# Performance work log

Measured on AMD Instinct MI355X. Metric: run time of the kernel, lower is better.

Reference implementation:

```python
import jax, jax.numpy as jnp
import numpy as np

D_MODEL = 1024
N_HEADS = 16
D_K = D_MODEL // N_HEADS
RANK = 16
LORA_SCALING = 32.0 / RANK  # alpha / rank = 2.0
LN_EPS = 1e-5


def _lora_linear(x, w, b, A, B):
    # torch nn.Linear: x @ w.T + b ; LoRA: (x @ A @ B) * scaling
    return x @ w.T + b + (x @ A @ B) * LORA_SCALING


def setup_inputs() -> dict:
    key = jax.random.key(0)
    ks = jax.random.split(key, 20)
    d = {}
    d['x'] = jax.random.normal(ks[0], (4, 1024, D_MODEL), dtype=jnp.float32)
    i = 1
    for p in ('q', 'k', 'v', 'o'):
        d[f'{p}_w'] = jax.random.normal(ks[i], (D_MODEL, D_MODEL), dtype=jnp.float32) * (1.0 / np.sqrt(D_MODEL)); i += 1
        d[f'{p}_b'] = jax.random.normal(ks[i], (D_MODEL,), dtype=jnp.float32) * 0.01; i += 1
        d[f'{p}_A'] = jax.random.normal(ks[i], (D_MODEL, RANK), dtype=jnp.float32) * 0.01; i += 1
        d[f'{p}_B'] = jax.random.normal(ks[i], (RANK, D_MODEL), dtype=jnp.float32) * 0.01; i += 1
    d['ln_g'] = jnp.ones((D_MODEL,), dtype=jnp.float32)
    d['ln_b'] = jnp.zeros((D_MODEL,), dtype=jnp.float32)
    return d


def reference(x, q_w, q_b, q_A, q_B, k_w, k_b, k_A, k_B,
              v_w, v_b, v_A, v_B, o_w, o_b, o_A, o_B, ln_g, ln_b):
    B, S, _ = x.shape
    # QKV projections with LoRA, reshape to [B, H, S, d_k]
    def split_heads(t):
        return t.reshape(B, S, N_HEADS, D_K).transpose(0, 2, 1, 3)
    Q = split_heads(_lora_linear(x, q_w, q_b, q_A, q_B))
    K = split_heads(_lora_linear(x, k_w, k_b, k_A, k_B))
    V = split_heads(_lora_linear(x, v_w, v_b, v_A, v_B))

    scores = jnp.einsum('bhqd,bhkd->bhqk', Q, K) / jnp.sqrt(jnp.float32(D_K))
    attn = jax.nn.softmax(scores, axis=-1)  # dropout is identity in eval
    ctx = jnp.einsum('bhqk,bhkd->bhqd', attn, V)
    ctx = ctx.transpose(0, 2, 1, 3).reshape(B, S, D_MODEL)

    out = _lora_linear(ctx, o_w, o_b, o_A, o_B)
    # residual + LayerNorm
    h = out + x
    mu = jnp.mean(h, axis=-1, keepdims=True)
    var = jnp.mean(jnp.square(h - mu), axis=-1, keepdims=True)
    normed = (h - mu) * jax.lax.rsqrt(var + LN_EPS) * ln_g + ln_b
    return normed, attn.mean(axis=1)
```

## Files before the change

### kernel.cpp

```cpp
#include <hip/hip_runtime.h>

#define DMODEL 1024
#define NHEADS 16
#define DHEAD  64
#define RANK   16
#define BATCH  4
#define SEQ    1024
#define MTOT   (BATCH*SEQ)
#define QSCALE 0.18033688011112042f

typedef __bf16 bf16;
typedef __bf16 bf16x8 __attribute__((ext_vector_type(8)));
typedef __bf16 bf16x4 __attribute__((ext_vector_type(4)));
typedef float  f32x4  __attribute__((ext_vector_type(4)));

__device__ __forceinline__ int swz128(int row, int byte_in_row) {
  int slot = byte_in_row >> 4;
  return row * 128 + (((slot ^ (row & 7)) << 4) | (byte_in_row & 15));
}

__device__ __forceinline__ void gll16(const void* g, void* l) {
  __builtin_amdgcn_global_load_lds((const __attribute__((address_space(1))) unsigned int*)g,
                                   (__attribute__((address_space(3))) unsigned int*)l, 16, 0, 0);
}

#define TRRD(lo, hi, base, o0, o1)                                   \
  asm volatile("ds_read_b64_tr_b16 %0, %2 offset:" #o0 "\n\t"        \
               "ds_read_b64_tr_b16 %1, %2 offset:" #o1               \
               : "=v"(lo), "=v"(hi) : "v"(base));

__global__ void prep_weff_kernel(
    const float* __restrict__ W0, const float* __restrict__ A0, const float* __restrict__ B0,
    const float* __restrict__ W1, const float* __restrict__ A1, const float* __restrict__ B1,
    const float* __restrict__ W2, const float* __restrict__ A2, const float* __restrict__ B2,
    const float* __restrict__ W3, const float* __restrict__ A3, const float* __restrict__ B3,
    bf16* __restrict__ out) {
  const int l = blockIdx.y;
  const float* W = l == 0 ? W0 : l == 1 ? W1 : l == 2 ? W2 : W3;
  const float* A = l == 0 ? A0 : l == 1 ? A1 : l == 2 ? A2 : A3;
  const float* Bm = l == 0 ? B0 : l == 1 ? B1 : l == 2 ? B2 : B3;
  out += (size_t)l * DMODEL * DMODEL;
  const int n = blockIdx.x;
  __shared__ float bsc[RANK];
  if (threadIdx.x < RANK) bsc[threadIdx.x] = Bm[threadIdx.x * DMODEL + n] * 2.0f;
  __syncthreads();
  float br[RANK];
#pragma unroll
  for (int r = 0; r < RANK; ++r) br[r] = bsc[r];
  for (int k0 = 0; k0 < DMODEL; k0 += 256) {
    int k = k0 + threadIdx.x;
    float acc = W[n * DMODEL + k];
    const float4* arow = (const float4*)(A + k * RANK);
#pragma unroll
    for (int r4 = 0; r4 < 4; ++r4) {
      float4 a = arow[r4];
      acc += a.x*br[r4*4+0] + a.y*br[r4*4+1] + a.z*br[r4*4+2] + a.w*br[r4*4+3];
    }
    out[n * DMODEL + k] = (bf16)acc;
  }
}

__global__ void cast_x_kernel(const float* __restrict__ x, bf16* __restrict__ xb) {
  int i = (blockIdx.x * blockDim.x + threadIdx.x) * 4;
  float4 v = *(const float4*)(x + i);
  bf16x4 o = { (bf16)v.x, (bf16)v.y, (bf16)v.z, (bf16)v.w };
  *(bf16x4*)(xb + i) = o;
}

__global__ __launch_bounds__(512) void gemm_qkv_kernel(
    const bf16* __restrict__ xb, const bf16* __restrict__ weff,
    const float* __restrict__ bq, const float* __restrict__ bk, const float* __restrict__ bv,
    bf16* __restrict__ Qb, bf16* __restrict__ Kb, bf16* __restrict__ Vb)
{
  __shared__ __align__(16) char sA[16384];
  __shared__ __align__(16) char sB[32768];
  const int tid = threadIdx.x, w = tid >> 6, lane = tid & 63;
  const int bid = blockIdx.x;
  const int nb = (bid & 7) * 48 + (bid >> 3);
  const int n0 = (nb % 12) * 256, m0 = (nb / 12) * 128;
  const int z = n0 >> 10;
  const float* bias = z == 0 ? bq : z == 1 ? bk : bv;
  bf16* outp = z == 0 ? Qb : (z == 1 ? Kb : Vb);
  const float scl = z == 0 ? QSCALE : 1.0f;
  const int wm = (w & 1) * 64, wn = (w >> 1) * 64;
  f32x4 acc[4][4] = {};

  const bf16* pA[2]; const bf16* pB[4]; char* lA[2]; char* lB[4];
#pragma unroll
  for (int i = 0; i < 2; ++i) {
    int ci = i * 8 + w;
    int row = ci * 8 + (lane >> 3);
    int ss = (lane & 7) ^ (row & 7);
    pA[i] = xb + (size_t)(m0 + row) * DMODEL + ss * 8;
    lA[i] = sA + ci * 1024;
  }
#pragma unroll
  for (int i = 0; i < 4; ++i) {
    int ci = i * 8 + w;
    int row = ci * 8 + (lane >> 3);
    int ss = (lane & 7) ^ (row & 7);
    pB[i] = weff + (size_t)(n0 + row) * DMODEL + ss * 8;
    lB[i] = sB + ci * 1024;
  }
  for (int kt = 0; kt < DMODEL / 64; ++kt) {
    const int kbase = kt * 64;
#pragma unroll
    for (int i = 0; i < 2; ++i) gll16(pA[i] + kbase, lA[i]);
#pragma unroll
    for (int i = 0; i < 4; ++i) gll16(pB[i] + kbase, lB[i]);
    __syncthreads();
#pragma unroll
    for (int ks = 0; ks < 2; ++ks) {
      bf16x8 af[4], bfg[4];
#pragma unroll
      for (int mi = 0; mi < 4; ++mi)
        af[mi] = *(const bf16x8*)(sA + swz128(wm + mi*16 + (lane & 15), ks*64 + (lane >> 4)*16));
#pragma unroll
      for (int ni = 0; ni < 4; ++ni)
        bfg[ni] = *(const bf16x8*)(sB + swz128(wn + ni*16 + (lane & 15), ks*64 + (lane >> 4)*16));
#pragma unroll
      for (int mi = 0; mi < 4; ++mi)
#pragma unroll
        for (int ni = 0; ni < 4; ++ni)
          acc[mi][ni] = __builtin_amdgcn_mfma_f32_16x16x32_bf16(af[mi], bfg[ni], acc[mi][ni], 0, 0, 0);
    }
    __syncthreads();
  }

#pragma unroll
  for (int mi = 0; mi < 4; ++mi) {
#pragma unroll
    for (int ni = 0; ni < 4; ++ni) {
      int col = n0 + wn + ni * 16 + (lane & 15);
      float bcol = bias[col & 1023];
      int h = (col >> 6) & 15, d = col & 63;
#pragma unroll
      for (int r = 0; r < 4; ++r) {
        int row = m0 + wm + mi * 16 + (lane >> 4) * 4 + r;
        float v = (acc[mi][ni][r] + bcol) * scl;
        int b = row >> 10, s = row & 1023;
        outp[(size_t)((b * NHEADS + h) * SEQ + s) * DHEAD + d] = (bf16)v;
      }
    }
  }
}

__device__ __forceinline__ void gemm_core64(
    const bf16* __restrict__ Ain, const bf16* __restrict__ Bin,
    char* sA, char* sB, int m0, int n0, f32x4 (&acc)[2][4]) {
  const int tid = threadIdx.x;
  const int w = tid >> 6, lane = tid & 63;
  const int wm = (w & 1) * 32, wn = (w >> 1) * 64;
  const bf16* pA[2]; char* lA[2];
  const bf16* pB[4]; char* lB[4];
#pragma unroll
  for (int i = 0; i < 2; ++i) {
    int chunk = i * 4 + w;
    int row = chunk * 8 + (lane >> 3);
    int ss = (lane & 7) ^ (row & 7);
    pA[i] = Ain + (size_t)(m0 + row) * DMODEL + ss * 8;
    lA[i] = sA + chunk * 1024;
  }
#pragma unroll
  for (int i = 0; i < 4; ++i) {
    int chunk = i * 4 + w;
    int row = chunk * 8 + (lane >> 3);
    int ss = (lane & 7) ^ (row & 7);
    pB[i] = Bin + (size_t)(n0 + row) * DMODEL + ss * 8;
    lB[i] = sB + chunk * 1024;
  }
  for (int kt = 0; kt < DMODEL / 64; ++kt) {
    const int kbase = kt * 64;
#pragma unroll
    for (int i = 0; i < 2; ++i) gll16(pA[i] + kbase, lA[i]);
#pragma unroll
    for (int i = 0; i < 4; ++i) gll16(pB[i] + kbase, lB[i]);
    __syncthreads();
#pragma unroll
    for (int ks = 0; ks < 2; ++ks) {
      bf16x8 af[2], bfg[4];
#pragma unroll
      for (int mi = 0; mi < 2; ++mi)
        af[mi] = *(const bf16x8*)(sA + swz128(wm + mi*16 + (lane & 15), ks*64 + (lane >> 4)*16));
#pragma unroll
      for (int ni = 0; ni < 4; ++ni)
        bfg[ni] = *(const bf16x8*)(sB + swz128(wn + ni*16 + (lane & 15), ks*64 + (lane >> 4)*16));
#pragma unroll
      for (int mi = 0; mi < 2; ++mi)
#pragma unroll
        for (int ni = 0; ni < 4; ++ni)
          acc[mi][ni] = __builtin_amdgcn_mfma_f32_16x16x32_bf16(af[mi], bfg[ni], acc[mi][ni], 0, 0, 0);
    }
    __syncthreads();
  }
}

__global__ __launch_bounds__(256) void gemm_o_kernel(
    const bf16* __restrict__ ctx, const bf16* __restrict__ weff,
    const float* __restrict__ bias, const float* __restrict__ resid,
    float* __restrict__ outf)
{
  __shared__ __align__(16) char sA[8192];
  __shared__ __align__(16) char sB[16384];
  const int tid = threadIdx.x, w = tid >> 6, lane = tid & 63;
  const int bid = blockIdx.x;
  const int nb = (bid & 7) * 64 + (bid >> 3);
  const int n0 = (nb & 7) * 128, m0 = (nb >> 3) * 64;
  const int wm = (w & 1) * 32, wn = (w >> 1) * 64;
  f32x4 acc[2][4] = {};
  gemm_core64(ctx, weff, sA, sB, m0, n0, acc);
#pragma unroll
  for (int mi = 0; mi < 2; ++mi) {
#pragma unroll
    for (int ni = 0; ni < 4; ++ni) {
      int col = n0 + wn + ni * 16 + (lane & 15);
      float bcol = bias[col];
#pragma unroll
      for (int r = 0; r < 4; ++r) {
        int row = m0 + wm + mi * 16 + (lane >> 4) * 4 + r;
        outf[(size_t)row * DMODEL + col] =
            acc[mi][ni][r] + bcol + resid[(size_t)row * DMODEL + col];
      }
    }
  }
}

__global__ __launch_bounds__(512) void flash_kernel(
    const bf16* __restrict__ Qb, const bf16* __restrict__ Kb, const bf16* __restrict__ Vb,
    bf16* __restrict__ ctx, float* __restrict__ lstat)
{
  __shared__ __align__(16) char sK[2 * 8192];
  __shared__ __align__(16) char sV[2 * 8192];
  __shared__ __align__(16) char sP[8 * 2048];
  const int tid = threadIdx.x, w = tid >> 6, lane = tid & 63;
  const int bid = blockIdx.x;
  const int nb = (bid & 7) * 64 + (bid >> 3);
  const int bh = nb >> 3;
  const int q0 = (nb & 7) * 128;
  const bf16* Qbase = Qb + (size_t)bh * SEQ * DHEAD;
  const bf16* Kbase = Kb + (size_t)bh * SEQ * DHEAD;
  const bf16* Vbase = Vb + (size_t)bh * SEQ * DHEAD;
  const int qw = q0 + w * 16;

  bf16x8 aq[2];
#pragma unroll
  for (int ks = 0; ks < 2; ++ks)
    aq[ks] = *(const bf16x8*)(Qbase + (size_t)(qw + (lane & 15)) * DHEAD + ks * 32 + (lane >> 4) * 8);

  const bf16* pK; const bf16* pV; int lKo; int lVo;
  {
    int ci = w;
    int rowK = ci * 8 + (lane >> 3);
    int ssK = (lane & 7) ^ (rowK & 7);
    pK = Kbase + (size_t)rowK * DHEAD + ssK * 8;
    lKo = ci * 1024;
    int kV = ci * 8 + ((lane >> 5) & 1) * 4 + ((lane >> 1) & 3);
    int dV = (((lane >> 3) & 3) << 4) + ((lane & 1) << 3);
    pV = Vbase + (size_t)kV * DHEAD + dV;
    lVo = ci * 1024;
  }

  char* sPw = sP + w * 2048;
  const unsigned pbase = (unsigned)(uintptr_t)sPw + ((lane >> 4) << 8) + ((lane & 15) << 3);
  const unsigned vbase0 = (unsigned)(uintptr_t)sV + ((lane >> 4) << 10) + ((lane & 15) << 3);
  char* pwr = sPw + ((lane >> 4) << 3) + (lane & 15) * 32;

  f32x4 cacc[4] = {};
  float lsum[4] = {0.f, 0.f, 0.f, 0.f};

  gll16(pK, sK + lKo);
  gll16(pV, sV + lVo);
  __syncthreads();

  for (int kt = 0; kt < SEQ / 64; ++kt) {
    const int cur = (kt & 1) << 13, nxt = cur ^ 8192;
    if (kt + 1 < SEQ / 64) {
      const size_t kofs = (size_t)((kt + 1) * 64) * DHEAD;
      gll16(pK + kofs, sK + nxt + lKo);
      gll16(pV + kofs, sV + nxt + lVo);
    }

    f32x4 sc[4] = {};
#pragma unroll
    for (int ks = 0; ks < 2; ++ks)
#pragma unroll
      for (int ni = 0; ni < 4; ++ni) {
        bf16x8 bk = *(const bf16x8*)(sK + cur + swz128(ni*16 + (lane & 15), ks*64 + (lane >> 4)*16));
        sc[ni] = __builtin_amdgcn_mfma_f32_16x16x32_bf16(aq[ks], bk, sc[ni], 0, 0, 0);
      }

#pragma unroll
    for (int ni = 0; ni < 4; ++ni) {
      float p0 = __builtin_amdgcn_exp2f(sc[ni][0]);
      float p1 = __builtin_amdgcn_exp2f(sc[ni][1]);
      float p2 = __builtin_amdgcn_exp2f(sc[ni][2]);
      float p3 = __builtin_amdgcn_exp2f(sc[ni][3]);
      lsum[0] += p0; lsum[1] += p1; lsum[2] += p2; lsum[3] += p3;
      bf16x4 pb = { (bf16)p0, (bf16)p1, (bf16)p2, (bf16)p3 };
      *(bf16x4*)(pwr + ni * 512) = pb;
    }
    asm volatile("s_waitcnt lgkmcnt(0)" ::: "memory");

    unsigned long long t0, t1, v0[4], v1[4];
    const unsigned vb = vbase0 + cur;
    TRRD(t0, t1, pbase, 0, 128)
    TRRD(v0[0], v1[0], vb, 0, 512)
    TRRD(v0[1], v1[1], vb, 128, 640)
    TRRD(v0[2], v1[2], vb, 256, 768)
    TRRD(v0[3], v1[3], vb, 384, 896)
    asm volatile("s_waitcnt lgkmcnt(0)" ::: "memory");
    __builtin_amdgcn_sched_barrier(0);
    {
      union { unsigned long long u[2]; bf16x8 v; } pu, vu;
      pu.u[0] = t0; pu.u[1] = t1;
#pragma unroll
      for (int ni = 0; ni < 4; ++ni) {
        vu.u[0] = v0[ni]; vu.u[1] = v1[ni];
        cacc[ni] = __builtin_amdgcn_mfma_f32_16x16x32_bf16(pu.v, vu.v, cacc[ni], 0, 0, 0);
      }
    }
    TRRD(t0, t1, pbase, 1024, 1152)
    TRRD(v0[0], v1[0], vb, 4096, 4608)
    TRRD(v0[1], v1[1], vb, 4224, 4736)
    TRRD(v0[2], v1[2], vb, 4352, 4864)
    TRRD(v0[3], v1[3], vb, 4480, 4992)
    asm volatile("s_waitcnt lgkmcnt(0)" ::: "memory");
    __builtin_amdgcn_sched_barrier(0);
    {
      union { unsigned long long u[2]; bf16x8 v; } pu, vu;
      pu.u[0] = t0; pu.u[1] = t1;
#pragma unroll
      for (int ni = 0; ni < 4; ++ni) {
        vu.u[0] = v0[ni]; vu.u[1] = v1[ni];
        cacc[ni] = __builtin_amdgcn_mfma_f32_16x16x32_bf16(pu.v, vu.v, cacc[ni], 0, 0, 0);
      }
    }
    __syncthreads();
  }

#pragma unroll
  for (int r = 0; r < 4; ++r) {
#pragma unroll
    for (int off = 1; off < 16; off <<= 1) lsum[r] += __shfl_xor(lsum[r], off);
  }

  const int b = bh >> 4, hh = bh & 15;
#pragma unroll
  for (int r = 0; r < 4; ++r) {
    float inv = __builtin_amdgcn_rcpf(lsum[r]);
    int qrow = qw + (lane >> 4) * 4 + r;
#pragma unroll
    for (int ni = 0; ni < 4; ++ni) {
      int d = ni * 16 + (lane & 15);
      ctx[(size_t)(b * SEQ + qrow) * DMODEL + hh * DHEAD + d] = (bf16)(cacc[ni][r] * inv);
    }
    if ((lane & 15) == 0) lstat[(size_t)bh * SEQ + qrow] = lsum[r];
  }
}

__global__ __launch_bounds__(256) void mean_kernel(
    const bf16* __restrict__ Qb, const bf16* __restrict__ Kb,
    const float* __restrict__ lstat, float* __restrict__ out2)
{
  __shared__ __align__(16) char sK[2 * 16384];
  const int tid = threadIdx.x, w = tid >> 6, lane = tid & 63;
  const int bid = blockIdx.x;
  const int nb2 = (bid & 7) * 64 + (bid >> 3);
  const int b = nb2 >> 7;
  const int q0 = ((nb2 >> 3) & 15) * 64, k0 = (nb2 & 7) * 128;
  const int qw = q0 + w * 16;
  size_t goff[4]; int lofs[4];
#pragma unroll
  for (int i = 0; i < 4; ++i) {
    int chunk = i * 4 + w;
    int row = chunk * 8 + (lane >> 3);
    int ss = (lane & 7) ^ (row & 7);
    goff[i] = (size_t)(k0 + row) * DHEAD + ss * 8;
    lofs[i] = chunk * 1024;
  }
  const bf16* Kb_b = Kb + (size_t)b * NHEADS * SEQ * DHEAD;
  const bf16* Qb_b = Qb + (size_t)b * NHEADS * SEQ * DHEAD;

  f32x4 macc[8] = {};
#pragma unroll
  for (int i = 0; i < 4; ++i) gll16(Kb_b + goff[i], sK + lofs[i]);
  asm volatile("s_waitcnt vmcnt(0)" ::: "memory");
  __syncthreads();

  for (int h = 0; h < NHEADS; ++h) {
    const int cur = (h & 1) << 14, nxt = cur ^ 16384;
    if (h + 1 < NHEADS) {
      const bf16* Kn = Kb_b + (size_t)(h + 1) * SEQ * DHEAD;
#pragma unroll
      for (int i = 0; i < 4; ++i) gll16(Kn + goff[i], sK + nxt + lofs[i]);
    }
    const bf16* Qbase = Qb_b + (size_t)h * SEQ * DHEAD;
    bf16x8 aq[2];
#pragma unroll
    for (int ks = 0; ks < 2; ++ks)
      aq[ks] = *(const bf16x8*)(Qbase + (size_t)(qw + (lane & 15)) * DHEAD
                                + ks * 32 + (lane >> 4) * 8);
    char* cK = sK + cur;
    f32x4 sc[8] = {};
#pragma unroll
    for (int ks = 0; ks < 2; ++ks)
#pragma unroll
      for (int ni = 0; ni < 8; ++ni) {
        bf16x8 bk = *(const bf16x8*)(cK + swz128(ni*16 + (lane & 15), ks*64 + (lane >> 4)*16));
        sc[ni] = __builtin_amdgcn_mfma_f32_16x16x32_bf16(aq[ks], bk, sc[ni], 0, 0, 0);
      }
    float lsc[4];
    const float* ls = lstat + ((size_t)(b * NHEADS + h)) * SEQ;
#pragma unroll
    for (int r = 0; r < 4; ++r)
      lsc[r] = 0.0625f * __builtin_amdgcn_rcpf(ls[qw + (lane >> 4)*4 + r]);
#pragma unroll
    for (int ni = 0; ni < 8; ++ni)
#pragma unroll
      for (int r = 0; r < 4; ++r)
        macc[ni][r] += __builtin_amdgcn_exp2f(sc[ni][r]) * lsc[r];
    asm volatile("s_waitcnt vmcnt(0)" ::: "memory");
    __syncthreads();
  }
#pragma unroll
  for (int r = 0; r < 4; ++r) {
    int qrow = qw + (lane >> 4) * 4 + r;
#pragma unroll
    for (int ni = 0; ni < 8; ++ni)
      out2[(size_t)(b * SEQ + qrow) * SEQ + k0 + ni * 16 + (lane & 15)] = macc[ni][r];
  }
}

__global__ __launch_bounds__(256) void ln_kernel(
    float* __restrict__ hb, const float* __restrict__ g,
    const float* __restrict__ bvec, float* __restrict__ out)
{
  const int row = blockIdx.x, t = threadIdx.x;
  float4 v = *(const float4*)(hb + (size_t)row * DMODEL + t * 4);
  float s = v.x + v.y + v.z + v.w;
  float s2 = v.x*v.x + v.y*v.y + v.z*v.z + v.w*v.w;
#pragma unroll
  for (int off = 32; off >= 1; off >>= 1) {
    s  += __shfl_down(s, off);
    s2 += __shfl_down(s2, off);
  }
  __shared__ float red[8];
  const int w = t >> 6;
  if ((t & 63) == 0) { red[w] = s; red[4 + w] = s2; }
  __syncthreads();
  if (t == 0) {
    red[0] = red[0] + red[1] + red[2] + red[3];
    red[4] = red[4] + red[5] + red[6] + red[7];
  }
  __syncthreads();
  float mu = red[0] * (1.0f / DMODEL);
  float var = red[4] * (1.0f / DMODEL) - mu * mu;
  float rs = rsqrtf(var + 1e-5f);
  float4 gv = *(const float4*)(g + t * 4);
  float4 bv = *(const float4*)(bvec + t * 4);
  float4 o;
  o.x = (v.x - mu) * rs * gv.x + bv.x;
  o.y = (v.y - mu) * rs * gv.y + bv.y;
  o.z = (v.z - mu) * rs * gv.z + bv.z;
  o.w = (v.w - mu) * rs * gv.w + bv.w;
  *(float4*)(out + (size_t)row * DMODEL + t * 4) = o;
}

extern "C" void kernel_launch(void* const* d_in, const int* in_sizes, int n_in,
                              void* d_out, int out_size, void* d_ws, size_t ws_size,
                              hipStream_t stream) {
  (void)in_sizes; (void)n_in; (void)out_size; (void)ws_size;
  const float* x = (const float*)d_in[0];
  const float* w_[4]  = {(const float*)d_in[1],  (const float*)d_in[5],
                         (const float*)d_in[9],  (const float*)d_in[13]};
  const float* b_[4]  = {(const float*)d_in[2],  (const float*)d_in[6],
                         (const float*)d_in[10], (const float*)d_in[14]};
  const float* A_[4]  = {(const float*)d_in[3],  (const float*)d_in[7],
                         (const float*)d_in[11], (const float*)d_in[15]};
  const float* Bm_[4] = {(const float*)d_in[4],  (const float*)d_in[8],
                         (const float*)d_in[12], (const float*)d_in[16]};
  const float* lng = (const float*)d_in[17];
  const float* lnb = (const float*)d_in[18];

  char* ws = (char*)d_ws;
  bf16* xb    = (bf16*)(ws);
  bf16* weff  = (bf16*)(ws + (8u  << 20));
  bf16* Qb    = (bf16*)(ws + (16u << 20));
  bf16* Kb    = (bf16*)(ws + (24u << 20));
  bf16* Vb    = (bf16*)(ws + (32u << 20));
  float* lstat = (float*)(ws + (40u << 20));
  bf16* ctx = xb;
  float* hbuf = (float*)d_out;
  float* out2 = (float*)d_out + (size_t)MTOT * DMODEL;

  prep_weff_kernel<<<dim3(DMODEL, 4), dim3(256), 0, stream>>>(
      w_[0], A_[0], Bm_[0], w_[1], A_[1], Bm_[1],
      w_[2], A_[2], Bm_[2], w_[3], A_[3], Bm_[3], weff);
  cast_x_kernel<<<dim3(MTOT * DMODEL / 1024), dim3(256), 0, stream>>>(x, xb);

  gemm_qkv_kernel<<<dim3(384), 512, 0, stream>>>(
      xb, weff, b_[0], b_[1], b_[2], Qb, Kb, Vb);

  flash_kernel<<<dim3(512), 512, 0, stream>>>(Qb, Kb, Vb, ctx, lstat);
  mean_kernel<<<dim3(512), 256, 0, stream>>>(Qb, Kb, lstat, out2);
  gemm_o_kernel<<<dim3(512), 256, 0, stream>>>(
      ctx, weff + 3u * DMODEL * DMODEL, b_[3], x, hbuf);
  ln_kernel<<<dim3(MTOT), 256, 0, stream>>>(hbuf, lng, lnb, hbuf);
}
```

Measured before the change: 137.2 us.

## Retile head-mean kernel to read K directly and raise MFMA wave priority

The head-averaged attention kernel drops its double-buffered LDS staging of K and its per-head barriers. Each wave now computes a 32x64 score tile, loading K fragments straight from global memory and reusing each K fragment across two Q row blocks. Separately, the attention kernel raises wave priority around its MFMA sections with s_setprio. The intent is to remove synchronisation and LDS overhead and to keep the matrix units busy, at the cost of more direct global/L2 traffic for K.

```diff
diff --git a/kernel.cpp b/kernel.cpp
--- a/kernel.cpp
+++ b/kernel.cpp
@@ -281,6 +281,7 @@
     }
 
     f32x4 sc[4] = {};
+    __builtin_amdgcn_s_setprio(1);
 #pragma unroll
     for (int ks = 0; ks < 2; ++ks)
 #pragma unroll
@@ -288,6 +289,7 @@
         bf16x8 bk = *(const bf16x8*)(sK + cur + swz128(ni*16 + (lane & 15), ks*64 + (lane >> 4)*16));
         sc[ni] = __builtin_amdgcn_mfma_f32_16x16x32_bf16(aq[ks], bk, sc[ni], 0, 0, 0);
       }
+    __builtin_amdgcn_s_setprio(0);
 
 #pragma unroll
     for (int ni = 0; ni < 4; ++ni) {
@@ -313,11 +315,13 @@
     {
       union { unsigned long long u[2]; bf16x8 v; } pu, vu;
       pu.u[0] = t0; pu.u[1] = t1;
+      __builtin_amdgcn_s_setprio(1);
 #pragma unroll
       for (int ni = 0; ni < 4; ++ni) {
         vu.u[0] = v0[ni]; vu.u[1] = v1[ni];
         cacc[ni] = __builtin_amdgcn_mfma_f32_16x16x32_bf16(pu.v, vu.v, cacc[ni], 0, 0, 0);
       }
+      __builtin_amdgcn_s_setprio(0);
     }
     TRRD(t0, t1, pbase, 1024, 1152)
     TRRD(v0[0], v1[0], vb, 4096, 4608)
@@ -329,11 +333,13 @@
     {
       union { unsigned long long u[2]; bf16x8 v; } pu, vu;
       pu.u[0] = t0; pu.u[1] = t1;
+      __builtin_amdgcn_s_setprio(1);
 #pragma unroll
       for (int ni = 0; ni < 4; ++ni) {
         vu.u[0] = v0[ni]; vu.u[1] = v1[ni];
         cacc[ni] = __builtin_amdgcn_mfma_f32_16x16x32_bf16(pu.v, vu.v, cacc[ni], 0, 0, 0);
       }
+      __builtin_amdgcn_s_setprio(0);
     }
     __syncthreads();
   }
@@ -362,73 +368,63 @@
     const bf16* __restrict__ Qb, const bf16* __restrict__ Kb,
     const float* __restrict__ lstat, float* __restrict__ out2)
 {
-  __shared__ __align__(16) char sK[2 * 16384];
   const int tid = threadIdx.x, w = tid >> 6, lane = tid & 63;
   const int bid = blockIdx.x;
-  const int nb2 = (bid & 7) * 64 + (bid >> 3);
-  const int b = nb2 >> 7;
-  const int q0 = ((nb2 >> 3) & 15) * 64, k0 = (nb2 & 7) * 128;
-  const int qw = q0 + w * 16;
-  size_t goff[4]; int lofs[4];
-#pragma unroll
-  for (int i = 0; i < 4; ++i) {
-    int chunk = i * 4 + w;
-    int row = chunk * 8 + (lane >> 3);
-    int ss = (lane & 7) ^ (row & 7);
-    goff[i] = (size_t)(k0 + row) * DHEAD + ss * 8;
-    lofs[i] = chunk * 1024;
-  }
+  const int nb = (bid & 7) * 64 + (bid >> 3);
+  const int b = nb >> 7;
+  const int nb2 = nb & 127;
+  const int q0 = (nb2 >> 4) * 128, k0 = (nb2 & 15) * 64;
+  const int qw = q0 + w * 32;
+  const bf16* Qb_b = Qb + (size_t)b * NHEADS * SEQ * DHEAD;
   const bf16* Kb_b = Kb + (size_t)b * NHEADS * SEQ * DHEAD;
-  const bf16* Qb_b = Qb + (size_t)b * NHEADS * SEQ * DHEAD;
-
-  f32x4 macc[8] = {};
-#pragma unroll
-  for (int i = 0; i < 4; ++i) gll16(Kb_b + goff[i], sK + lofs[i]);
-  asm volatile("s_waitcnt vmcnt(0)" ::: "memory");
-  __syncthreads();
-
+  const float* ls_b = lstat + (size_t)b * NHEADS * SEQ;
+
+  f32x4 macc[2][4] = {};
   for (int h = 0; h < NHEADS; ++h) {
-    const int cur = (h & 1) << 14, nxt = cur ^ 16384;
-    if (h + 1 < NHEADS) {
-      const bf16* Kn = Kb_b + (size_t)(h + 1) * SEQ * DHEAD;
-#pragma unroll
-      for (int i = 0; i < 4; ++i) gll16(Kn + goff[i], sK + nxt + lofs[i]);
-    }
     const bf16* Qbase = Qb_b + (size_t)h * SEQ * DHEAD;
-    bf16x8 aq[2];
+    const bf16* Kbase = Kb_b + (size_t)h * SEQ * DHEAD;
+    bf16x8 aq[2][2];
+#pragma unroll
+    for (int mi = 0; mi < 2; ++mi)
+#pragma unroll
+      for (int ks = 0; ks < 2; ++ks)
+        aq[mi][ks] = *(const bf16x8*)(Qbase + (size_t)(qw + mi*16 + (lane & 15)) * DHEAD
+                                      + ks * 32 + (lane >> 4) * 8);
+    f32x4 sc[2][4] = {};
 #pragma unroll
     for (int ks = 0; ks < 2; ++ks)
-      aq[ks] = *(const bf16x8*)(Qbase + (size_t)(qw + (lane & 15)) * DHEAD
-                                + ks * 32 + (lane >> 4) * 8);
-    char* cK = sK + cur;
-    f32x4 sc[8] = {};
-#pragma unroll
-    for (int ks = 0; ks < 2; ++ks)
-#pragma unroll
-      for (int ni = 0; ni < 8; ++ni) {
-        bf16x8 bk = *(const bf16x8*)(cK + swz128(ni*16 + (lane & 15), ks*64 + (lane >> 4)*16));
-        sc[ni] = __builtin_amdgcn_mfma_f32_16x16x32_bf16(aq[ks], bk, sc[ni], 0, 0, 0);
+#pragma unroll
+      for (int ni = 0; ni < 4; ++ni) {
+        bf16x8 bk = *(const bf16x8*)(Kbase + (size_t)(k0 + ni*16 + (lane & 15)) * DHEAD
+                                     + ks * 32 + (lane >> 4) * 8);
+#pragma unroll
+        for (int mi = 0; mi < 2; ++mi)
+          sc[mi][ni] = __builtin_amdgcn_mfma_f32_16x16x32_bf16(aq[mi][ks], bk, sc[mi][ni], 0, 0, 0);
       }
-    float lsc[4];
-    const float* ls = lstat + ((size_t)(b * NHEADS + h)) * SEQ;
-#pragma unroll
-    for (int r = 0; r < 4; ++r)
-      lsc[r] = 0.0625f * __builtin_amdgcn_rcpf(ls[qw + (lane >> 4)*4 + r]);
-#pragma unroll
-    for (int ni = 0; ni < 8; ++ni)
+    const float* ls = ls_b + (size_t)h * SEQ;
+    float lsc[2][4];
+#pragma unroll
+    for (int mi = 0; mi < 2; ++mi)
 #pragma unroll
       for (int r = 0; r < 4; ++r)
-        macc[ni][r] += __builtin_amdgcn_exp2f(sc[ni][r]) * lsc[r];
-    asm volatile("s_waitcnt vmcnt(0)" ::: "memory");
-    __syncthreads();
-  }
-#pragma unroll
-  for (int r = 0; r < 4; ++r) {
-    int qrow = qw + (lane >> 4) * 4 + r;
-#pragma unroll
-    for (int ni = 0; ni < 8; ++ni)
-      out2[(size_t)(b * SEQ + qrow) * SEQ + k0 + ni * 16 + (lane & 15)] = macc[ni][r];
-  }
+        lsc[mi][r] = 0.0625f * __builtin_amdgcn_rcpf(ls[qw + mi*16 + (lane >> 4)*4 + r]);
+#pragma unroll
+    for (int mi = 0; mi < 2; ++mi)
+#pragma unroll
+      for (int ni = 0; ni < 4; ++ni)
+#pragma unroll
+        for (int r = 0; r < 4; ++r)
+          macc[mi][ni][r] += __builtin_amdgcn_exp2f(sc[mi][ni][r]) * lsc[mi][r];
+  }
+#pragma unroll
+  for (int mi = 0; mi < 2; ++mi)
+#pragma unroll
+    for (int r = 0; r < 4; ++r) {
+      int qrow = qw + mi*16 + (lane >> 4) * 4 + r;
+#pragma unroll
+      for (int ni = 0; ni < 4; ++ni)
+        out2[(size_t)(b * SEQ + qrow) * SEQ + k0 + ni * 16 + (lane & 15)] = macc[mi][ni][r];
+    }
 }
 
 __global__ __launch_bounds__(256) void ln_kernel(
```

Result: slower. 161.7 us (+17.8%).
